# Optimization experiments

Measured on AMD Instinct MI355X. Metric: run time of the kernel, lower is better.

The kernel has to match this reference:

```python
import jax, jax.numpy as jnp
import numpy as np


def setup_inputs() -> dict:
    key = jax.random.key(0)
    k1, k2 = jax.random.split(key)
    B, S = 2048, 512
    # effective pixel intensity samples (positive), per pixel over time
    it_eff = jax.random.uniform(k1, (B, S), minval=0.05, maxval=1.05, dtype=jnp.float32)
    # strictly increasing sample timestamps, dt ~ 1e-4 s
    dts = jax.random.uniform(k2, (B, S), minval=5e-5, maxval=1.5e-4, dtype=jnp.float32)
    ts = jnp.cumsum(dts, axis=1)
    return {
        "it_eff": it_eff,
        "ts": ts,
        # buffer (no softplus): tau_in * it_eff product constant
        "tau_in_it_eff_prod": jnp.float32(1e-4),
        # raw (pre-softplus) learned parameters, softplus(raw) = actual value
        "tau_mil_raw": jnp.float32(-9.0),    # tau_mil_it_eff_prod ~ 1.2e-4
        "A_amp_inv_raw": jnp.float32(-3.0),  # A_amp ~ 20.6
        "A_loop_inv_raw": jnp.float32(-4.0), # A_loop ~ 55
        "tau_out_raw": jnp.float32(-8.0),    # tau_out ~ 3.4e-4 s
        "tau_sf_raw": jnp.float32(-9.0),     # tau_sf ~ 1.2e-4 s
        "tau_diff_raw": jnp.float32(-10.0),  # tau_diff ~ 4.5e-5 s
    }


def _forward(it_eff, ts, tau_in_it_eff_prod, tau_mil_raw, A_amp_inv_raw,
             A_loop_inv_raw, tau_out_raw, tau_sf_raw, tau_diff_raw):
    sp = jax.nn.softplus
    tau_mil_prod = sp(tau_mil_raw)
    A_amp = 1.0 / sp(A_amp_inv_raw)
    A_loop = 1.0 / sp(A_loop_inv_raw)
    tau_out = sp(tau_out_raw)
    omega_c_sf = 1.0 / sp(tau_sf_raw)
    omega_c_diff = 1.0 / sp(tau_diff_raw)

    B, S = it_eff.shape
    K = S - 1
    u = jnp.log(it_eff)                      # effective log-intensity input
    dt = ts[:, 1:] - ts[:, :-1]              # [B, K]

    # Linearize NLTI photoreceptor LPF at steady state = next input sample
    I_ss = it_eff[:, 1:]                     # [B, K]
    tau_in = tau_in_it_eff_prod / I_ss
    tau_mil = tau_mil_prod / I_ss
    denom = (tau_in + tau_mil) * tau_out
    two_zeta_omega_n = (tau_in + tau_out + (A_amp + 1.0) * tau_mil) / denom
    omega_n_sq = (A_loop + 1.0) / denom

    # Augmented matrix for FOH discretization: expm([[A*dt, B*dt, 0],[0,0,1],[0,0,0]])
    # top-left -> Ad, col 4 -> Gamma1, col 5 -> Gamma2 (FOH ramp integral / dt)
    em = jnp.zeros((B, K, 6, 6), dtype=it_eff.dtype)
    em = (em.at[..., 0, 0].set(-two_zeta_omega_n * dt)
            .at[..., 0, 1].set(-omega_n_sq * dt)
            .at[..., 1, 0].set(dt)
            .at[..., 2, 1].set(omega_c_sf * dt)
            .at[..., 2, 2].set(-omega_c_sf * dt)
            .at[..., 3, 2].set(omega_c_diff * dt)
            .at[..., 3, 3].set(-omega_c_diff * dt)
            .at[..., 0, 4].set(omega_n_sq * dt)
            .at[..., 4, 5].set(1.0))
    ms = jax.vmap(jax.scipy.linalg.expm)(em.reshape(-1, 6, 6)).reshape(B, K, 6, 6)
    Ad = ms[..., :4, :4]                     # [B, K, 4, 4]
    G1 = ms[..., :4, 4]                      # [B, K, 4]
    G2 = ms[..., :4, 5]                      # [B, K, 4]
    Bd = G1 - G2                             # coeff of u[k]
    Bt = G2                                  # coeff of u[k+1] (FOH)

    # steady-state initial state at u[0]: x = [0, u0, u0, u0]
    u0 = u[:, 0]
    x0 = jnp.stack([jnp.zeros_like(u0), u0, u0, u0], axis=-1)  # [B, 4]

    def step(x, inp):
        Ad_k, Bd_k, Bt_k, u_k, u_k1 = inp
        x_new = (jnp.einsum('bij,bj->bi', Ad_k, x)
                 + Bd_k * u_k[:, None] + Bt_k * u_k1[:, None])
        return x_new, x_new[:, 3]            # diff-amp LPF output state

    xs = (jnp.moveaxis(Ad, 1, 0), jnp.moveaxis(Bd, 1, 0), jnp.moveaxis(Bt, 1, 0),
          u[:, :-1].T, u[:, 1:].T)
    _, ys = jax.lax.scan(step, x0, xs)       # ys: [K, B]
    y = jnp.concatenate([u0[:, None], ys.T], axis=1)  # [B, S]
    return y


def reference(it_eff, ts, tau_in_it_eff_prod, tau_mil_raw, A_amp_inv_raw,
              A_loop_inv_raw, tau_out_raw, tau_sf_raw, tau_diff_raw):
    return _forward(it_eff, ts, tau_in_it_eff_prod, tau_mil_raw, A_amp_inv_raw,
                    A_loop_inv_raw, tau_out_raw, tau_sf_raw, tau_diff_raw)
```

## Files before the change

kernel.cpp:

```cpp
#include <hip/hip_runtime.h>
#include <math.h>

namespace {
constexpr int BB  = 2048;
constexpr int SS  = 512;
constexpr int TPB = 128;
constexpr int NSQ = 4;
constexpr float SCV = 0.0625f;
constexpr float LOG2E = 1.44269504f;
}

__device__ __forceinline__ float frcp(float x) { return __builtin_amdgcn_rcpf(x); }
__device__ __forceinline__ float frsq(float x) { return __builtin_amdgcn_rsqf(x); }
__device__ __forceinline__ float flog(float x) {
    return __builtin_amdgcn_logf(x) * 0.69314718056f;
}
__device__ __forceinline__ float fexp2(float x) {
    return __builtin_amdgcn_exp2f(x);
}

struct Aff {
    float a00, a01, a10, a11;
    float a20, a21, a22;
    float a30, a31, a32, a33;
    float c0, c1, c2, c3;
};

__device__ __forceinline__ Aff aff_identity() {
    Aff r;
    r.a00 = 1.f; r.a01 = 0.f; r.a10 = 0.f; r.a11 = 1.f;
    r.a20 = 0.f; r.a21 = 0.f; r.a22 = 1.f;
    r.a30 = 0.f; r.a31 = 0.f; r.a32 = 0.f; r.a33 = 1.f;
    r.c0 = 0.f; r.c1 = 0.f; r.c2 = 0.f; r.c3 = 0.f;
    return r;
}

struct Osc { float a00, a01, a10, a11, c0, c1; };

__device__ __forceinline__ Osc osc_compose(const Osc& s, const Osc& f) {
    Osc r;
    r.a00 = s.a00*f.a00 + s.a01*f.a10;
    r.a01 = s.a00*f.a01 + s.a01*f.a11;
    r.a10 = s.a10*f.a00 + s.a11*f.a10;
    r.a11 = s.a10*f.a01 + s.a11*f.a11;
    r.c0  = s.a00*f.c0 + s.a01*f.c1 + s.c0;
    r.c1  = s.a10*f.c0 + s.a11*f.c1 + s.c1;
    return r;
}
__device__ __forceinline__ Osc osc_shfl_up(const Osc& a, int d) {
    Osc r;
    r.a00 = __shfl_up(a.a00, d, 64); r.a01 = __shfl_up(a.a01, d, 64);
    r.a10 = __shfl_up(a.a10, d, 64); r.a11 = __shfl_up(a.a11, d, 64);
    r.c0  = __shfl_up(a.c0,  d, 64); r.c1  = __shfl_up(a.c1,  d, 64);
    return r;
}
__device__ __forceinline__ Osc osc_sel(const Osc& p, bool ok) {
    Osc r;
    r.a00 = ok ? p.a00 : 1.f; r.a01 = ok ? p.a01 : 0.f;
    r.a10 = ok ? p.a10 : 0.f; r.a11 = ok ? p.a11 : 1.f;
    r.c0  = ok ? p.c0  : 0.f; r.c1  = ok ? p.c1  : 0.f;
    return r;
}
__device__ __forceinline__ void osc_apply(const Osc& m, float& v0, float& v1) {
    const float y0 = m.a00*v0 + m.a01*v1 + m.c0;
    const float y1 = m.a10*v0 + m.a11*v1 + m.c1;
    v0 = y0; v1 = y1;
}

struct Low { float l00, l10, l11, c0, c1; };

__device__ __forceinline__ Low low_compose(const Low& s, const Low& f) {
    Low r;
    r.l00 = s.l00*f.l00;
    r.l10 = s.l10*f.l00 + s.l11*f.l10;
    r.l11 = s.l11*f.l11;
    r.c0  = fmaf(s.l00, f.c0, s.c0);
    r.c1  = fmaf(s.l10, f.c0, fmaf(s.l11, f.c1, s.c1));
    return r;
}
__device__ __forceinline__ Low low_shfl_up(const Low& a, int d) {
    Low r;
    r.l00 = __shfl_up(a.l00, d, 64); r.l10 = __shfl_up(a.l10, d, 64);
    r.l11 = __shfl_up(a.l11, d, 64);
    r.c0  = __shfl_up(a.c0,  d, 64); r.c1  = __shfl_up(a.c1,  d, 64);
    return r;
}
__device__ __forceinline__ Low low_sel(const Low& p, bool ok) {
    Low r;
    r.l00 = ok ? p.l00 : 1.f; r.l10 = ok ? p.l10 : 0.f;
    r.l11 = ok ? p.l11 : 1.f;
    r.c0  = ok ? p.c0  : 0.f; r.c1  = ok ? p.c1  : 0.f;
    return r;
}
__device__ __forceinline__ void low_apply(const Low& m, float& x2, float& x3) {
    const float y2 = fmaf(m.l00, x2, m.c0);
    const float y3 = m.l10*x2 + m.l11*x3 + m.c1;
    x2 = y2; x3 = y3;
}

__device__ __forceinline__ Aff make_step(
    float Iss, float dt, float uk, float uk1,
    float rK, float AK, float tau_out, float aprod,
    float wsf, float wdf, float rwsf, float rwdf, float CWD,
    float wsfL, float wdfL)
{
    const float a   = fmaf(tau_out, Iss, aprod) * rK;
    const float w2  = AK * Iss;
    const float iw  = frsq(w2);
    const float w   = w2 * iw;

    const float dts = dt * SCV;
    const float tt  = -a * dts;
    const float f10 =  w * dts;
    const float f01 = -f10;
    const float dd  = f10 * f10;
    const float f21 =  wsf * dts;
    const float f22 = -f21;
    const float f32 =  wdf * dts;
    const float f33 = -f32;

    const float K1 = f21 * f10;
    float al = 1.0f/6.0f, be = 1.0f;
    float c00 = 0.0f, c01 = f21 * (1.0f/6.0f), c10 = 0.0f, c11 = 0.0f;
#pragma unroll
    for (int m = 5; m >= 1; --m) {
        const float rm = 1.0f / (float)m;
        const float q00 = K1*al  + f22*c00;
        const float q01 = f21*be + f22*c01;
        const float q10 = f32*c00 + f33*c10;
        const float q11 = f32*c01 + f33*c11;
        const float arm = al * rm;
        const float na  = fmaf(al, tt, be) * rm;
        const float nb  = fmaf(-arm, dd, 1.0f);
        al = na; be = nb;
        c00 = q00*rm; c01 = q01*rm; c10 = q10*rm; c11 = q11*rm;
    }
    float t00 = fmaf(al, tt, be);
    float t01 = al * f01;
    float t10 = al * f10;
    float t11 = be;

    float l00 = fexp2(wsfL * dts);
    float l11 = fexp2(wdfL * dts);
    float l10 = CWD * (l00 - l11);

#pragma unroll
    for (int i = 0; i < NSQ; ++i) {
        const float p00 = t00*t00 + t01*t10;
        const float p01 = t00*t01 + t01*t11;
        const float p10 = t10*t00 + t11*t10;
        const float p11 = t10*t01 + t11*t11;
        const float q00 = c00*t00 + c01*t10 + l00*c00;
        const float q01 = c00*t01 + c01*t11 + l00*c01;
        const float q10 = c10*t00 + c11*t10 + l10*c00 + l11*c10;
        const float q11 = c10*t01 + c11*t11 + l10*c01 + l11*c11;
        const float m00 = l00*l00;
        const float m10 = l10*l00 + l11*l10;
        const float m11 = l11*l11;
        t00 = p00; t01 = p01; t10 = p10; t11 = p11;
        c00 = q00; c01 = q01; c10 = q10; c11 = q11;
        l00 = m00; l10 = m10; l11 = m11;
    }

    const float aw  = a * iw;
    const float rdt = frcp(dt);
    const float rF  = iw * rdt;
    const float rS  = rwsf * rdt;
    const float rD  = rwdf * rdt;
    const float wS  = w * rwsf;
    const float wD  = w * rwdf;
    const float g0u = w * dt;

    const float y0 = t10;
    const float y1 = -fmaf(aw, t10, t00 - 1.0f);
    const float y2 = fmaf(-wS, c00, y1);
    const float y3 = fmaf(-wD, c10, y2);
    const float s0 = y0 - g0u;
    const float z0 = y1 * rF;
    const float z1 = -fmaf(aw, z0, rF * s0);
    const float z2 = fmaf(-y2, rS, z1);
    const float z3 = fmaf(-y3, rD, z2);

    Aff r;
    r.a00 = t00;      r.a01 = w * t01;
    r.a10 = t10 * iw; r.a11 = t11;
    r.a20 = c00 * iw; r.a21 = c01; r.a22 = l00;
    r.a30 = c10 * iw; r.a31 = c11; r.a32 = l10; r.a33 = l11;
    const float G10 = w * y0, G20 = w * z0;
    const float du = uk1 - uk;
    r.c0 = fmaf(G10, uk, G20 * du);
    r.c1 = fmaf(y1,  uk, z1 * du);
    r.c2 = fmaf(y2,  uk, z2 * du);
    r.c3 = fmaf(y3,  uk, z3 * du);
    return r;
}

__global__ __launch_bounds__(TPB) void pbw_kernel(
    const float* __restrict__ it_eff,
    const float* __restrict__ ts,
    const float* __restrict__ p_tin_prod,
    const float* __restrict__ p_tmil_raw,
    const float* __restrict__ p_aamp_raw,
    const float* __restrict__ p_aloop_raw,
    const float* __restrict__ p_tout_raw,
    const float* __restrict__ p_tsf_raw,
    const float* __restrict__ p_tdiff_raw,
    float* __restrict__ out)
{
    __shared__ float swcA[6];
    __shared__ float swcB[5];

    const int b = blockIdx.x;
    const int t = threadIdx.x;
    const int lane = t & 63;
    const int wv = t >> 6;

    const float tin_prod  = p_tin_prod[0];
    const float tmil_prod = log1pf(expf(p_tmil_raw[0]));
    const float Aamp1     = 1.0f / log1pf(expf(p_aamp_raw[0])) + 1.0f;
    const float Aloop1    = 1.0f / log1pf(expf(p_aloop_raw[0])) + 1.0f;
    const float tau_out   = log1pf(expf(p_tout_raw[0]));
    const float sp_sf     = log1pf(expf(p_tsf_raw[0]));
    const float sp_df     = log1pf(expf(p_tdiff_raw[0]));
    const float wsf       = 1.0f / sp_sf;
    const float wdf       = 1.0f / sp_df;
    const float CWD       = wdf / (wdf - wsf);
    const float sprod = tin_prod + tmil_prod;
    const float aprod = fmaf(Aamp1, tmil_prod, tin_prod);
    const float rK    = 1.0f / (sprod * tau_out);
    const float AK    = Aloop1 * rK;
    const float wsfL  = -wsf * LOG2E;
    const float wdfL  = -wdf * LOG2E;

    const float* rowI = it_eff + (size_t)b * SS;
    const float* rowT = ts     + (size_t)b * SS;

    const int k0 = 4 * t;
    const float4 I4 = *(const float4*)(rowI + k0);
    const float4 T4 = *(const float4*)(rowT + k0);
    const bool last = (t == TPB - 1);
    const float I_4 = last ? 1.0f : rowI[k0 + 4];
    const float T_4 = last ? (T4.w + 1e-4f) : rowT[k0 + 4];

    const float u_0 = flog(I4.x);
    const float u_1 = flog(I4.y);
    const float u_2 = flog(I4.z);
    const float u_3 = flog(I4.w);
    const float u_4 = flog(I_4);
    const float u0  = flog(rowI[0]);

    Aff m0 = make_step(I4.y, T4.y - T4.x, u_0, u_1,
                       rK, AK, tau_out, aprod, wsf, wdf, sp_sf, sp_df, CWD,
                       wsfL, wdfL);
    Aff m1 = make_step(I4.z, T4.z - T4.y, u_1, u_2,
                       rK, AK, tau_out, aprod, wsf, wdf, sp_sf, sp_df, CWD,
                       wsfL, wdfL);
    Aff m2 = make_step(I4.w, T4.w - T4.z, u_2, u_3,
                       rK, AK, tau_out, aprod, wsf, wdf, sp_sf, sp_df, CWD,
                       wsfL, wdfL);
    Aff m3 = make_step(I_4, T_4 - T4.w, u_3, u_4,
                       rK, AK, tau_out, aprod, wsf, wdf, sp_sf, sp_df, CWD,
                       wsfL, wdfL);
    if (last) m3 = aff_identity();

    const Osc s0 = {m0.a00, m0.a01, m0.a10, m0.a11, m0.c0, m0.c1};
    const Osc s1 = {m1.a00, m1.a01, m1.a10, m1.a11, m1.c0, m1.c1};
    const Osc s2 = {m2.a00, m2.a01, m2.a10, m2.a11, m2.c0, m2.c1};
    const Osc s3 = {m3.a00, m3.a01, m3.a10, m3.a11, m3.c0, m3.c1};

    Osc oc = osc_compose(osc_compose(s3, s2), osc_compose(s1, s0));
#pragma unroll
    for (int d = 1; d < 64; d <<= 1) {
        Osc p = osc_shfl_up(oc, d);
        p = osc_sel(p, lane >= d);
        oc = osc_compose(oc, p);
    }
    if (wv == 0 && lane == 63) {
        swcA[0]=oc.a00; swcA[1]=oc.a01; swcA[2]=oc.a10; swcA[3]=oc.a11;
        swcA[4]=oc.c0;  swcA[5]=oc.c1;
    }
    __syncthreads();

    float v0 = 0.0f, v1 = u0;
    if (wv == 1) {
        Osc wm = {swcA[0], swcA[1], swcA[2], swcA[3], swcA[4], swcA[5]};
        osc_apply(wm, v0, v1);
    }
    Osc oex = osc_shfl_up(oc, 1);
    oex = osc_sel(oex, lane >= 1);
    osc_apply(oex, v0, v1);

    const float va0 = v0, vb0 = v1;
    osc_apply(s0, v0, v1); const float va1 = v0, vb1 = v1;
    osc_apply(s1, v0, v1); const float va2 = v0, vb2 = v1;
    osc_apply(s2, v0, v1); const float va3 = v0, vb3 = v1;

    const Low b0 = {m0.a22, m0.a32, m0.a33,
                    m0.a20*va0 + m0.a21*vb0 + m0.c2,
                    m0.a30*va0 + m0.a31*vb0 + m0.c3};
    const Low b1 = {m1.a22, m1.a32, m1.a33,
                    m1.a20*va1 + m1.a21*vb1 + m1.c2,
                    m1.a30*va1 + m1.a31*vb1 + m1.c3};
    const Low b2 = {m2.a22, m2.a32, m2.a33,
                    m2.a20*va2 + m2.a21*vb2 + m2.c2,
                    m2.a30*va2 + m2.a31*vb2 + m2.c3};
    const Low b3 = {m3.a22, m3.a32, m3.a33,
                    m3.a20*va3 + m3.a21*vb3 + m3.c2,
                    m3.a30*va3 + m3.a31*vb3 + m3.c3};

    Low lc = low_compose(low_compose(b3, b2), low_compose(b1, b0));
#pragma unroll
    for (int d = 1; d < 64; d <<= 1) {
        Low p = low_shfl_up(lc, d);
        p = low_sel(p, lane >= d);
        lc = low_compose(lc, p);
    }
    if (wv == 0 && lane == 63) {
        swcB[0]=lc.l00; swcB[1]=lc.l10; swcB[2]=lc.l11;
        swcB[3]=lc.c0;  swcB[4]=lc.c1;
    }
    __syncthreads();

    float x2 = u0, x3 = u0;
    if (wv == 1) {
        Low wm = {swcB[0], swcB[1], swcB[2], swcB[3], swcB[4]};
        low_apply(wm, x2, x3);
    }
    Low lex = low_shfl_up(lc, 1);
    lex = low_sel(lex, lane >= 1);
    low_apply(lex, x2, x3);

    const float y_0 = x3;
    low_apply(b0, x2, x3); const float y_1 = x3;
    low_apply(b1, x2, x3); const float y_2 = x3;
    low_apply(b2, x2, x3); const float y_3 = x3;

    float4* po = (float4*)(out + (size_t)b * SS);
    po[t] = make_float4(y_0, y_1, y_2, y_3);
}

extern "C" void kernel_launch(void* const* d_in, const int* in_sizes, int n_in,
                              void* d_out, int out_size, void* d_ws, size_t ws_size,
                              hipStream_t stream) {
    const float* it_eff = (const float*)d_in[0];
    const float* ts     = (const float*)d_in[1];
    const float* p2 = (const float*)d_in[2];
    const float* p3 = (const float*)d_in[3];
    const float* p4 = (const float*)d_in[4];
    const float* p5 = (const float*)d_in[5];
    const float* p6 = (const float*)d_in[6];
    const float* p7 = (const float*)d_in[7];
    const float* p8 = (const float*)d_in[8];
    float* out = (float*)d_out;

    pbw_kernel<<<dim3(BB), dim3(TPB), 0, stream>>>(
        it_eff, ts, p2, p3, p4, p5, p6, p7, p8, out);
}
```

Measured before the change: 88.14 us.

## Use 256 threads per row with two timesteps per thread

Doubles threads per block from 128 to 256 so each thread handles two timesteps instead of four, with a four-wave block prefix. Cross-wave carries are stored per wave in shared memory and applied serially by each later wave. This shortens each thread's serial work and register footprint but adds more waves doing the same 6-step shuffle scans, plus a small serial loop over earlier waves' carries.

```diff
diff --git a/kernel.cpp b/kernel.cpp
--- a/kernel.cpp
+++ b/kernel.cpp
@@ -4,7 +4,7 @@
 namespace {
 constexpr int BB  = 2048;
 constexpr int SS  = 512;
-constexpr int TPB = 128;
+constexpr int TPB = 256;
 constexpr int NSQ = 4;
 constexpr float SCV = 0.0625f;
 constexpr float LOG2E = 1.44269504f;
@@ -207,8 +207,8 @@
     const float* __restrict__ p_tdiff_raw,
     float* __restrict__ out)
 {
-    __shared__ float swcA[6];
-    __shared__ float swcB[5];
+    __shared__ float swcA[4 * 6];
+    __shared__ float swcB[4 * 5];
 
     const int b = blockIdx.x;
     const int t = threadIdx.x;
@@ -235,55 +235,47 @@
     const float* rowI = it_eff + (size_t)b * SS;
     const float* rowT = ts     + (size_t)b * SS;
 
-    const int k0 = 4 * t;
-    const float4 I4 = *(const float4*)(rowI + k0);
-    const float4 T4 = *(const float4*)(rowT + k0);
+    const int k0 = 2 * t;
+    const float2 I01 = *(const float2*)(rowI + k0);
+    const float2 T01 = *(const float2*)(rowT + k0);
     const bool last = (t == TPB - 1);
-    const float I_4 = last ? 1.0f : rowI[k0 + 4];
-    const float T_4 = last ? (T4.w + 1e-4f) : rowT[k0 + 4];
-
-    const float u_0 = flog(I4.x);
-    const float u_1 = flog(I4.y);
-    const float u_2 = flog(I4.z);
-    const float u_3 = flog(I4.w);
-    const float u_4 = flog(I_4);
+    const float I_2 = last ? 1.0f : rowI[k0 + 2];
+    const float T_2 = last ? (T01.y + 1e-4f) : rowT[k0 + 2];
+
+    const float u_0 = flog(I01.x);
+    const float u_1 = flog(I01.y);
+    const float u_2 = flog(I_2);
     const float u0  = flog(rowI[0]);
 
-    Aff m0 = make_step(I4.y, T4.y - T4.x, u_0, u_1,
+    Aff m0 = make_step(I01.y, T01.y - T01.x, u_0, u_1,
                        rK, AK, tau_out, aprod, wsf, wdf, sp_sf, sp_df, CWD,
                        wsfL, wdfL);
-    Aff m1 = make_step(I4.z, T4.z - T4.y, u_1, u_2,
+    Aff m1 = make_step(I_2, T_2 - T01.y, u_1, u_2,
                        rK, AK, tau_out, aprod, wsf, wdf, sp_sf, sp_df, CWD,
                        wsfL, wdfL);
-    Aff m2 = make_step(I4.w, T4.w - T4.z, u_2, u_3,
-                       rK, AK, tau_out, aprod, wsf, wdf, sp_sf, sp_df, CWD,
-                       wsfL, wdfL);
-    Aff m3 = make_step(I_4, T_4 - T4.w, u_3, u_4,
-                       rK, AK, tau_out, aprod, wsf, wdf, sp_sf, sp_df, CWD,
-                       wsfL, wdfL);
-    if (last) m3 = aff_identity();
+    if (last) m1 = aff_identity();
 
     const Osc s0 = {m0.a00, m0.a01, m0.a10, m0.a11, m0.c0, m0.c1};
     const Osc s1 = {m1.a00, m1.a01, m1.a10, m1.a11, m1.c0, m1.c1};
-    const Osc s2 = {m2.a00, m2.a01, m2.a10, m2.a11, m2.c0, m2.c1};
-    const Osc s3 = {m3.a00, m3.a01, m3.a10, m3.a11, m3.c0, m3.c1};
-
-    Osc oc = osc_compose(osc_compose(s3, s2), osc_compose(s1, s0));
+
+    Osc oc = osc_compose(s1, s0);
 #pragma unroll
     for (int d = 1; d < 64; d <<= 1) {
         Osc p = osc_shfl_up(oc, d);
         p = osc_sel(p, lane >= d);
         oc = osc_compose(oc, p);
     }
-    if (wv == 0 && lane == 63) {
-        swcA[0]=oc.a00; swcA[1]=oc.a01; swcA[2]=oc.a10; swcA[3]=oc.a11;
-        swcA[4]=oc.c0;  swcA[5]=oc.c1;
+    if (lane == 63) {
+        float* dst = &swcA[wv * 6];
+        dst[0]=oc.a00; dst[1]=oc.a01; dst[2]=oc.a10; dst[3]=oc.a11;
+        dst[4]=oc.c0;  dst[5]=oc.c1;
     }
     __syncthreads();
 
     float v0 = 0.0f, v1 = u0;
-    if (wv == 1) {
-        Osc wm = {swcA[0], swcA[1], swcA[2], swcA[3], swcA[4], swcA[5]};
+    for (int j = 0; j < wv; ++j) {
+        const float* m = &swcA[j * 6];
+        Osc wm = {m[0], m[1], m[2], m[3], m[4], m[5]};
         osc_apply(wm, v0, v1);
     }
     Osc oex = osc_shfl_up(oc, 1);
@@ -292,8 +284,6 @@
 
     const float va0 = v0, vb0 = v1;
     osc_apply(s0, v0, v1); const float va1 = v0, vb1 = v1;
-    osc_apply(s1, v0, v1); const float va2 = v0, vb2 = v1;
-    osc_apply(s2, v0, v1); const float va3 = v0, vb3 = v1;
 
     const Low b0 = {m0.a22, m0.a32, m0.a33,
                     m0.a20*va0 + m0.a21*vb0 + m0.c2,
@@ -301,29 +291,25 @@
     const Low b1 = {m1.a22, m1.a32, m1.a33,
                     m1.a20*va1 + m1.a21*vb1 + m1.c2,
                     m1.a30*va1 + m1.a31*vb1 + m1.c3};
-    const Low b2 = {m2.a22, m2.a32, m2.a33,
-                    m2.a20*va2 + m2.a21*vb2 + m2.c2,
-                    m2.a30*va2 + m2.a31*vb2 + m2.c3};
-    const Low b3 = {m3.a22, m3.a32, m3.a33,
-                    m3.a20*va3 + m3.a21*vb3 + m3.c2,
-                    m3.a30*va3 + m3.a31*vb3 + m3.c3};
-
-    Low lc = low_compose(low_compose(b3, b2), low_compose(b1, b0));
+
+    Low lc = low_compose(b1, b0);
 #pragma unroll
     for (int d = 1; d < 64; d <<= 1) {
         Low p = low_shfl_up(lc, d);
         p = low_sel(p, lane >= d);
         lc = low_compose(lc, p);
     }
-    if (wv == 0 && lane == 63) {
-        swcB[0]=lc.l00; swcB[1]=lc.l10; swcB[2]=lc.l11;
-        swcB[3]=lc.c0;  swcB[4]=lc.c1;
+    if (lane == 63) {
+        float* dst = &swcB[wv * 5];
+        dst[0]=lc.l00; dst[1]=lc.l10; dst[2]=lc.l11;
+        dst[3]=lc.c0;  dst[4]=lc.c1;
     }
     __syncthreads();
 
     float x2 = u0, x3 = u0;
-    if (wv == 1) {
-        Low wm = {swcB[0], swcB[1], swcB[2], swcB[3], swcB[4]};
+    for (int j = 0; j < wv; ++j) {
+        const float* m = &swcB[j * 5];
+        Low wm = {m[0], m[1], m[2], m[3], m[4]};
         low_apply(wm, x2, x3);
     }
     Low lex = low_shfl_up(lc, 1);
@@ -332,11 +318,9 @@
 
     const float y_0 = x3;
     low_apply(b0, x2, x3); const float y_1 = x3;
-    low_apply(b1, x2, x3); const float y_2 = x3;
-    low_apply(b2, x2, x3); const float y_3 = x3;
-
-    float4* po = (float4*)(out + (size_t)b * SS);
-    po[t] = make_float4(y_0, y_1, y_2, y_3);
+
+    float2* po = (float2*)(out + (size_t)b * SS);
+    po[t] = make_float2(y_0, y_1);
 }
 
 extern "C" void kernel_launch(void* const* d_in, const int* in_sizes, int n_in,
```

After: 93.43 us. 1.06x slower.
